# Kernel optimization log

Hardware: AMD Instinct MI355X
Metric: run time of the kernel (lower is better)

## Reference

```python
import jax, jax.numpy as jnp
import numpy as np

WS = (8, 8, 8)          # window_size (d, h, w) -- all equal
N_TOK = WS[0] * WS[1] * WS[2]   # 512
DIM = 192
HEADS = 6
HEAD_DIM = DIM // HEADS  # 32
B_ = 64                  # num_windows * batch (batch = 1)


def _build_rel_coords_table():
    # matches torch: meshgrid of arange(-(w-1), w) per axis, normalized, *8, signed log2
    r = np.arange(-(WS[0] - 1), WS[0], dtype=np.float32)
    tab = np.stack(np.meshgrid(r, r, r, indexing='ij'), axis=-1)[None]  # (1,15,15,15,3)
    tab = tab / (WS[0] - 1)
    tab = tab * 8.0
    tab = np.sign(tab) * np.log2(np.abs(tab) + 1.0) / np.log2(8.0)
    return tab.astype(np.float32)


def _build_rel_pos_index():
    c = np.arange(WS[0])
    coords = np.stack(np.meshgrid(c, c, c, indexing='ij'))          # (3, 8, 8, 8)
    flat = coords.reshape(3, -1)                                     # (3, N)
    rel = flat[:, :, None] - flat[:, None, :]                        # (3, N, N)
    rel = rel.transpose(1, 2, 0).copy()                              # (N, N, 3)
    rel += WS[0] - 1
    rel[:, :, 0] *= (2 * WS[1] - 1) * (2 * WS[2] - 1)
    rel[:, :, 1] *= 2 * WS[2] - 1
    return rel.sum(-1).astype(np.int32)                              # (N, N)


def setup_inputs() -> dict:
    key = jax.random.key(0)
    ks = jax.random.split(key, 8)
    x = jax.random.normal(ks[0], (B_, N_TOK, DIM), dtype=jnp.float32)
    # 0 / -inf style additive mask (use large negative finite for stability)
    m = jax.random.uniform(ks[1], (B_, N_TOK, N_TOK))
    mask = jnp.where(m < 0.1, jnp.float32(-1e4), jnp.float32(0.0))
    w_qkv = jax.random.normal(ks[2], (3 * DIM, DIM), dtype=jnp.float32) * (DIM ** -0.5)
    q_bias = jnp.zeros((DIM,), jnp.float32)
    v_bias = jnp.zeros((DIM,), jnp.float32)
    cpb_w1 = jax.random.normal(ks[3], (512, 3), dtype=jnp.float32) * 0.3
    cpb_b1 = jnp.zeros((512,), jnp.float32)
    cpb_w2 = jax.random.normal(ks[4], (HEADS, 512), dtype=jnp.float32) * 0.05
    rel_coords_table = jnp.asarray(_build_rel_coords_table())
    rel_pos_index = jnp.asarray(_build_rel_pos_index())
    return {"x": x, "mask": mask, "w_qkv": w_qkv, "q_bias": q_bias,
            "v_bias": v_bias, "cpb_w1": cpb_w1, "cpb_b1": cpb_b1,
            "cpb_w2": cpb_w2, "rel_coords_table": rel_coords_table,
            "rel_pos_index": rel_pos_index}


def reference(x, mask, w_qkv, q_bias, v_bias, cpb_w1, cpb_b1, cpb_w2,
              rel_coords_table, rel_pos_index):
    Bw, N, C = x.shape
    H, D = HEADS, HEAD_DIM
    # qkv projection with bias = cat(q_bias, zeros, v_bias)
    qkv_bias = jnp.concatenate([q_bias, jnp.zeros_like(v_bias), v_bias])
    qkv = x @ w_qkv.T + qkv_bias                       # (Bw, N, 3C)
    qkv = qkv.reshape(Bw, N, 3, H, D).transpose(2, 0, 3, 1, 4)
    q, k, v = qkv[0], qkv[1], qkv[2]                   # (Bw, H, N, D)
    # continuous position bias MLP: 3 -> 512 -> H
    tab = rel_coords_table.reshape(-1, 3)              # (3375, 3)
    tab = jax.nn.relu(tab @ cpb_w1.T + cpb_b1) @ cpb_w2.T  # (3375, H)
    bias = tab[rel_pos_index.reshape(-1)].reshape(N, N, H)
    bias = 16.0 * jax.nn.sigmoid(bias.transpose(2, 0, 1))  # (H, N, N)
    # SDPA with additive mask (standard 1/sqrt(D) scaling, as in forward_flash)
    scale = jnp.float32(1.0 / np.sqrt(D))
    scores = jnp.einsum('bhnd,bhmd->bhnm', q, k) * scale
    scores = scores + mask[:, None, :, :] + bias[None]
    attn = jax.nn.softmax(scores, axis=-1)
    out = jnp.einsum('bhnm,bhmd->bhnd', attn, v)       # (Bw, H, N, D)
    return out
```

## Files before the change

kernel.cpp:

```cpp
#include <hip/hip_runtime.h>
#include <hip/hip_bf16.h>


typedef __bf16 bf16x8 __attribute__((ext_vector_type(8)));
typedef __bf16 bf16x4v __attribute__((ext_vector_type(4)));
typedef float  f32x4  __attribute__((ext_vector_type(4)));
typedef _Float16 f16x4 __attribute__((ext_vector_type(4)));
typedef _Float16 f16x8 __attribute__((ext_vector_type(8)));
typedef unsigned uint2v __attribute__((ext_vector_type(2)));
typedef int int4v __attribute__((ext_vector_type(4)));
typedef unsigned long long u64;

#define LOG2E 1.4426950408889634f

__device__ __forceinline__ bf16x8 cvt2_bf16x8(f32x4 a, f32x4 b) {
  bf16x8 r;
  r[0] = (__bf16)a[0]; r[1] = (__bf16)a[1]; r[2] = (__bf16)a[2]; r[3] = (__bf16)a[3];
  r[4] = (__bf16)b[0]; r[5] = (__bf16)b[1]; r[6] = (__bf16)b[2]; r[7] = (__bf16)b[3];
  return r;
}

__device__ __forceinline__ unsigned pack2bf(float a, float b) {
  unsigned short ua = __builtin_bit_cast(unsigned short, (__bf16)a);
  unsigned short ub = __builtin_bit_cast(unsigned short, (__bf16)b);
  return (unsigned)ua | ((unsigned)ub << 16);
}

__device__ __forceinline__ bf16x8 frag_from_words(unsigned w0, unsigned w1,
                                                  unsigned w2, unsigned w3) {
  union { unsigned u[4]; bf16x8 v; } f;
  f.u[0] = w0; f.u[1] = w1; f.u[2] = w2; f.u[3] = w3;
  return f.v;
}

#define PREP_MB    2048
#define PREP_WCONV 108
#define PREP_CPB   3375
#define PREP_GRID  (PREP_MB + PREP_WCONV + PREP_CPB)

__global__ __launch_bounds__(256) void prep_kernel(
    const float* __restrict__ w, __bf16* __restrict__ wbf,
    const float* __restrict__ table, const float* __restrict__ w1,
    const float* __restrict__ b1, const float* __restrict__ w2,
    float* __restrict__ tab6,
    const float* __restrict__ m, u64* __restrict__ bits)
{
  __shared__ float red[4][6];
  int blk = blockIdx.x;
  if (blk < PREP_MB) {
    int li8 = threadIdx.x & 7;
    for (size_t t = (size_t)blk * 256 + threadIdx.x;
         t < 2097152ull; t += (size_t)PREP_MB * 256) {
      const float* mp = m + t * 8;
      f32x4 v0 = *(const f32x4*)mp;
      f32x4 v1 = *(const f32x4*)(mp + 4);
      unsigned byte =
          (v0[0] == 0.f ? 1u : 0u)  | (v0[1] == 0.f ? 2u : 0u) |
          (v0[2] == 0.f ? 4u : 0u)  | (v0[3] == 0.f ? 8u : 0u) |
          (v1[0] == 0.f ? 16u : 0u) | (v1[1] == 0.f ? 32u : 0u) |
          (v1[2] == 0.f ? 64u : 0u) | (v1[3] == 0.f ? 128u : 0u);
      u64 part = (u64)byte << (8 * li8);
      part |= __shfl_xor(part, 1);
      part |= __shfl_xor(part, 2);
      part |= __shfl_xor(part, 4);
      if (li8 == 0) {
        int w_ = (int)(t >> 3);
        int b = w_ >> 12, i = (w_ >> 3) & 511, jw = w_ & 7;
        bits[(((size_t)b * 8 + jw) << 9) + i] = part;
      }
    }
  } else if (blk < PREP_MB + PREP_WCONV) {
    int t = (blk - PREP_MB) * 256 + threadIdx.x;
    f32x4 v = *(const f32x4*)(w + (size_t)t * 4);
    bf16x4v o;
    o[0] = (__bf16)v[0]; o[1] = (__bf16)v[1]; o[2] = (__bf16)v[2]; o[3] = (__bf16)v[3];
    *(bf16x4v*)(wbf + (size_t)t * 4) = o;
  } else {
    int p = blk - PREP_MB - PREP_WCONV;
    float c0 = table[p * 3 + 0], c1 = table[p * 3 + 1], c2 = table[p * 3 + 2];
    float acc[6] = {0.f, 0.f, 0.f, 0.f, 0.f, 0.f};
#pragma unroll
    for (int jj = 0; jj < 2; ++jj) {
      int j = threadIdx.x + jj * 256;
      float hv = w1[j * 3 + 0] * c0 + w1[j * 3 + 1] * c1 + w1[j * 3 + 2] * c2 + b1[j];
      hv = fmaxf(hv, 0.0f);
#pragma unroll
      for (int t = 0; t < 6; ++t) acc[t] += w2[t * 512 + j] * hv;
    }
#pragma unroll
    for (int t = 0; t < 6; ++t) {
      acc[t] += __shfl_xor(acc[t], 1);
      acc[t] += __shfl_xor(acc[t], 2);
      acc[t] += __shfl_xor(acc[t], 4);
      acc[t] += __shfl_xor(acc[t], 8);
      acc[t] += __shfl_xor(acc[t], 16);
      acc[t] += __shfl_xor(acc[t], 32);
    }
    int wave = threadIdx.x >> 6;
    if ((threadIdx.x & 63) == 0)
#pragma unroll
      for (int t = 0; t < 6; ++t) red[wave][t] = acc[t];
    __syncthreads();
    if (threadIdx.x < 6) {
      int t = threadIdx.x;
      float s = red[0][t] + red[1][t] + red[2][t] + red[3][t];
      float sig = 16.0f / (1.0f + expf(-s));
      tab6[p * 8 + t] = sig * LOG2E;
    }
  }
}

#define MID_QKV  1024
#define MID_BIAS 342
#define MID_GRID (MID_QKV + MID_BIAS)

__global__ __launch_bounds__(192) void mid_kernel(
    const float* __restrict__ x,
    const __bf16* __restrict__ wbf,
    const float* __restrict__ qb,
    const float* __restrict__ vb,
    __bf16* __restrict__ Qo,
    __bf16* __restrict__ Ko,
    __bf16* __restrict__ Vt,
    const int* __restrict__ relidx,
    const float* __restrict__ tab6,
    _Float16* __restrict__ biasH)
{
  __shared__ __bf16 tile[2][32][72];
  if (blockIdx.x >= MID_QKV) {
    for (int q4 = (blockIdx.x - MID_QKV) * 192 + threadIdx.x; q4 < 65536;
         q4 += MID_BIAS * 192) {
      int ij = q4 * 4;
      int i = ij >> 9, p = ij & 511;
      int jblk = p >> 6, g = (p >> 4) & 3, kf = (p >> 2) & 3;
      int j = (jblk << 6) + kf * 16 + g * 4;
      int4v idx4 = *(const int4v*)(relidx + (i << 9) + j);
      float val[6][4];
#pragma unroll
      for (int u = 0; u < 4; ++u) {
        f32x4 lo = *(const f32x4*)(tab6 + (size_t)idx4[u] * 8);
        f32x4 hi = *(const f32x4*)(tab6 + (size_t)idx4[u] * 8 + 4);
        val[0][u] = lo[0]; val[1][u] = lo[1]; val[2][u] = lo[2];
        val[3][u] = lo[3]; val[4][u] = hi[0]; val[5][u] = hi[1];
      }
#pragma unroll
      for (int t6 = 0; t6 < 6; ++t6) {
        f16x4 o = {(_Float16)val[t6][0], (_Float16)val[t6][1],
                   (_Float16)val[t6][2], (_Float16)val[t6][3]};
        *(f16x4*)(biasH + (size_t)t6 * 262144 + ij) = o;
      }
    }
    return;
  }
  const float CQ = 0.17677669529663687f * LOG2E;
  int lane = threadIdx.x & 63, wave = threadIdx.x >> 6;
  int g = lane >> 4, li = lane & 15;
  int rowbase = blockIdx.x * 32;
  int b = rowbase >> 9, nbase = rowbase & 511;

  bf16x8 a[2][6];
#pragma unroll
  for (int mm = 0; mm < 2; ++mm)
#pragma unroll
    for (int k = 0; k < 6; ++k) {
      const float* xp = x + (size_t)(rowbase + mm * 16 + li) * 192 + k * 32 + 8 * g;
      f32x4 x0 = *(const f32x4*)xp;
      f32x4 x1 = *(const f32x4*)(xp + 4);
      a[mm][k] = cvt2_bf16x8(x0, x1);
    }

  for (int ncl = 0; ncl < 3; ++ncl) {
    int nc = wave * 3 + ncl;
    f32x4 acc[2][4];
#pragma unroll
    for (int n = 0; n < 4; ++n) {
      int r = nc * 64 + n * 16 + li;
      float bb = 0.0f;
      if (r < 192) bb = qb[r];
      else if (r >= 384) bb = vb[r - 384];
      f32x4 v = {bb, bb, bb, bb};
      acc[0][n] = v; acc[1][n] = v;
    }
#pragma unroll
    for (int k = 0; k < 6; ++k) {
#pragma unroll
      for (int n = 0; n < 4; ++n) {
        bf16x8 bf = *(const bf16x8*)(wbf + (size_t)(nc * 64 + n * 16 + li) * 192 + k * 32 + 8 * g);
        acc[0][n] = __builtin_amdgcn_mfma_f32_16x16x32_bf16(a[0][k], bf, acc[0][n], 0, 0, 0);
        acc[1][n] = __builtin_amdgcn_mfma_f32_16x16x32_bf16(a[1][k], bf, acc[1][n], 0, 0, 0);
      }
    }
    if (wave < 2) {
      float scale = (wave == 0) ? CQ : 1.0f;
#pragma unroll
      for (int n = 0; n < 4; ++n)
#pragma unroll
        for (int mm = 0; mm < 2; ++mm)
#pragma unroll
          for (int t = 0; t < 4; ++t)
            tile[wave][mm * 16 + 4 * g + t][n * 16 + li] = (__bf16)(acc[mm][n][t] * scale);
      int tok = lane & 31, hh = lane >> 5;
      int h = (nc * 2 + hh) % 6;
      __bf16* base = (wave == 0) ? Qo : Ko;
      __bf16* dst = base + ((size_t)(b * 6 + h) * 512 + nbase + tok) * 32;
#pragma unroll
      for (int kq = 0; kq < 4; ++kq)
        *(bf16x8*)(dst + kq * 8) = *(const bf16x8*)&tile[wave][tok][hh * 32 + kq * 8];
    } else {
#pragma unroll
      for (int n = 0; n < 4; ++n) {
        int rr = nc * 64 + n * 16 + li - 384, h = rr >> 5, d = rr & 31;
#pragma unroll
        for (int mm = 0; mm < 2; ++mm) {
          int nn = nbase + mm * 16 + 4 * g;
          bf16x4v pk;
#pragma unroll
          for (int t = 0; t < 4; ++t) pk[t] = (__bf16)acc[mm][n][t];
          *(bf16x4v*)(Vt + ((size_t)(b * 6 + h) * 32 + d) * 512 + nn) = pk;
        }
      }
    }
  }
}

__global__ __launch_bounds__(256, 3) void attn_kernel(
    const u64* __restrict__ bits,
    const _Float16* __restrict__ biasH,
    const __bf16* __restrict__ Qw,
    const __bf16* __restrict__ Kw,
    const __bf16* __restrict__ Vt,
    float* __restrict__ out)
{
  int hw = blockIdx.x;
  int xcd = hw & 7, seq = hw >> 3;
  int h = seq >> 4;
  int r = seq & 15;
  int b = xcd * 8 + (r >> 1);
  int qt = r & 1;
  int lane = threadIdx.x & 63, wave = threadIdx.x >> 6;
  int g = lane >> 4, li = lane & 15;
  int qbase = qt * 256 + wave * 64;
  int bh = b * 6 + h;
  int gsh = 4 * g;

  const __bf16* Qb = Qw + (size_t)bh * 16384;
  const __bf16* Kb = Kw + (size_t)bh * 16384;
  const __bf16* Vb = Vt + (size_t)bh * 16384;
  const _Float16* biasb = biasH + (size_t)h * 262144 + g * 16;
  const u64* bitsb = bits + (size_t)b * 4096;

  bf16x8 qfrag[4];
#pragma unroll
  for (int qf = 0; qf < 4; ++qf)
    qfrag[qf] = *(const bf16x8*)(Qb + (qbase + qf * 16 + li) * 32 + 8 * g);

  f32x4 oacc[4][2] = {};
  float l_part[4] = {0.f, 0.f, 0.f, 0.f};

  for (int kb = 0; kb < 8; ++kb) {
    int j64 = kb * 64;
    u64 mb[4];
#pragma unroll
    for (int qf = 0; qf < 4; ++qf)
      mb[qf] = bitsb[(kb << 9) + qbase + qf * 16 + li] >> gsh;
    bf16x8 kfr[4];
#pragma unroll
    for (int kf = 0; kf < 4; ++kf)
      kfr[kf] = *(const bf16x8*)(Kb + (j64 + kf * 16 + li) * 32 + 8 * g);
    bf16x8 vfr[2][2];
#pragma unroll
    for (int df = 0; df < 2; ++df)
#pragma unroll
      for (int c = 0; c < 2; ++c)
        vfr[df][c] = *(const bf16x8*)(Vb + (df * 16 + li) * 512 + j64 + c * 32 + 8 * g);
    f16x8 hv8[4][2];
#pragma unroll
    for (int qf = 0; qf < 4; ++qf) {
      const _Float16* bp = biasb + (size_t)(qbase + qf * 16 + li) * 512 + j64;
      hv8[qf][0] = *(const f16x8*)(bp);
      hv8[qf][1] = *(const f16x8*)(bp + 8);
    }

#pragma unroll
    for (int c = 0; c < 2; ++c) {
      unsigned lo[4][2], hi[4][2];
#pragma unroll
      for (int kfl = 0; kfl < 2; ++kfl) {
        int kf = c * 2 + kfl;
        const int hsel = kf >> 1, hoff = (kf & 1) * 4;
#pragma unroll
        for (int qf = 0; qf < 4; ++qf) {
          f16x8 hb = hv8[qf][hsel];
          f32x4 ci = {(float)hb[hoff], (float)hb[hoff + 1],
                      (float)hb[hoff + 2], (float)hb[hoff + 3]};
          f32x4 s = __builtin_amdgcn_mfma_f32_16x16x32_bf16(kfr[kf], qfrag[qf], ci, 0, 0, 0);
          unsigned nib = (unsigned)(mb[qf] >> (kf * 16)) & 15u;
          float p0 = (nib & 1u) ? __builtin_amdgcn_exp2f(s[0]) : 0.0f;
          float p1 = (nib & 2u) ? __builtin_amdgcn_exp2f(s[1]) : 0.0f;
          float p2 = (nib & 4u) ? __builtin_amdgcn_exp2f(s[2]) : 0.0f;
          float p3 = (nib & 8u) ? __builtin_amdgcn_exp2f(s[3]) : 0.0f;
          l_part[qf] += (p0 + p1) + (p2 + p3);
          lo[qf][kfl] = pack2bf(p0, p1);
          hi[qf][kfl] = pack2bf(p2, p3);
        }
      }
#pragma unroll
      for (int qf = 0; qf < 4; ++qf) {
        uint2v sl = __builtin_amdgcn_permlane32_swap(lo[qf][0], lo[qf][1], 0, 0);
        uint2v wl = __builtin_amdgcn_permlane16_swap(sl.x, sl.y, 0, 0);
        uint2v sh = __builtin_amdgcn_permlane32_swap(hi[qf][0], hi[qf][1], 0, 0);
        uint2v wh = __builtin_amdgcn_permlane16_swap(sh.x, sh.y, 0, 0);
        bf16x8 pf = frag_from_words(wl.x, wh.x, wl.y, wh.y);
#pragma unroll
        for (int df = 0; df < 2; ++df)
          oacc[qf][df] = __builtin_amdgcn_mfma_f32_16x16x32_bf16(vfr[df][c], pf, oacc[qf][df], 0, 0, 0);
      }
    }
  }

#pragma unroll
  for (int qf = 0; qf < 4; ++qf) {
    float l = l_part[qf];
    l += __shfl_xor(l, 16);
    l += __shfl_xor(l, 32);
    float linv = 1.0f / l;
#pragma unroll
    for (int df = 0; df < 2; ++df) {
      float* op = out + ((size_t)bh * 512 + qbase + qf * 16 + li) * 32 + df * 16 + 4 * g;
      f32x4 r2 = oacc[qf][df] * linv;
      *(f32x4*)op = r2;
    }
  }
}

extern "C" void kernel_launch(void* const* d_in, const int* in_sizes, int n_in,
                              void* d_out, int out_size, void* d_ws, size_t ws_size,
                              hipStream_t stream) {
  const float* x    = (const float*)d_in[0];
  const float* mask = (const float*)d_in[1];
  const float* wqkv = (const float*)d_in[2];
  const float* qb   = (const float*)d_in[3];
  const float* vb   = (const float*)d_in[4];
  const float* w1   = (const float*)d_in[5];
  const float* b1   = (const float*)d_in[6];
  const float* w2   = (const float*)d_in[7];
  const float* tbl  = (const float*)d_in[8];
  const int*   ridx = (const int*)d_in[9];
  float* out = (float*)d_out;

  char* ws = (char*)d_ws;
  float*    tab6  = (float*)(ws);
  _Float16* biasH = (_Float16*)(ws + 131072);
  u64*      bits  = (u64*)(ws + 131072 + 3145728);
  __bf16*   wbf   = (__bf16*)(ws + 131072 + 3145728 + 2097152);
  __bf16*   Q     = (__bf16*)(ws + 131072 + 3145728 + 2097152 + 262144);
  __bf16*   K     = Q + (size_t)64 * 6 * 512 * 32;
  __bf16*   Vt    = K + (size_t)64 * 6 * 512 * 32;

  prep_kernel<<<PREP_GRID, 256, 0, stream>>>(wqkv, wbf, tbl, w1, b1, w2, tab6,
                                             mask, bits);
  mid_kernel<<<MID_GRID, 192, 0, stream>>>(x, wbf, qb, vb, Q, K, Vt,
                                           ridx, tab6, biasH);
  attn_kernel<<<768, 256, 0, stream>>>(bits, biasH, Q, K, Vt, out);
}
```

Before: 119.9 us.

## Compute softmax row sums via MFMA with ones and branchless bitmask masking

Replaces the per-lane scalar accumulation of softmax denominators (and the final cross-lane shuffles) with an extra MFMA that multiplies the bf16 probability fragment by a ones matrix, so row sums come out of the matrix unit. Mask handling switches from conditional selects on a 64-bit word to sign-extended bit masks ANDed into the exp2 results, using 32-bit halves. It also raises wave priority around the compute loop with s_setprio. This trades VALU adds and shuffles for one more MFMA per fragment, and the denominators are now summed from bf16-rounded probabilities, which slightly changes numerics.

New measurement: 111.3 us (median of 3 runs). 1.08x faster.

```diff
diff --git a/kernel.cpp b/kernel.cpp
--- a/kernel.cpp
+++ b/kernel.cpp
@@ -254,15 +254,23 @@
   for (int qf = 0; qf < 4; ++qf)
     qfrag[qf] = *(const bf16x8*)(Qb + (qbase + qf * 16 + li) * 32 + 8 * g);
 
+  union { unsigned short us[8]; bf16x8 v; } onesu;
+#pragma unroll
+  for (int i = 0; i < 8; ++i) onesu.us[i] = 0x3F80;
+  bf16x8 ones = onesu.v;
+
   f32x4 oacc[4][2] = {};
-  float l_part[4] = {0.f, 0.f, 0.f, 0.f};
+  f32x4 lacc[4] = {};
 
   for (int kb = 0; kb < 8; ++kb) {
     int j64 = kb * 64;
-    u64 mb[4];
-#pragma unroll
-    for (int qf = 0; qf < 4; ++qf)
-      mb[qf] = bitsb[(kb << 9) + qbase + qf * 16 + li] >> gsh;
+    unsigned mbl[4], mbh[4];
+#pragma unroll
+    for (int qf = 0; qf < 4; ++qf) {
+      u64 m64 = bitsb[(kb << 9) + qbase + qf * 16 + li] >> gsh;
+      mbl[qf] = (unsigned)m64;
+      mbh[qf] = (unsigned)(m64 >> 32);
+    }
     bf16x8 kfr[4];
 #pragma unroll
     for (int kf = 0; kf < 4; ++kf)
@@ -281,6 +289,7 @@
       hv8[qf][1] = *(const f16x8*)(bp + 8);
     }
 
+    __builtin_amdgcn_s_setprio(1);
 #pragma unroll
     for (int c = 0; c < 2; ++c) {
       unsigned lo[4][2], hi[4][2];
@@ -288,18 +297,26 @@
       for (int kfl = 0; kfl < 2; ++kfl) {
         int kf = c * 2 + kfl;
         const int hsel = kf >> 1, hoff = (kf & 1) * 4;
+        const int bb0 = (kf & 1) * 16;
 #pragma unroll
         for (int qf = 0; qf < 4; ++qf) {
           f16x8 hb = hv8[qf][hsel];
           f32x4 ci = {(float)hb[hoff], (float)hb[hoff + 1],
                       (float)hb[hoff + 2], (float)hb[hoff + 3]};
           f32x4 s = __builtin_amdgcn_mfma_f32_16x16x32_bf16(kfr[kf], qfrag[qf], ci, 0, 0, 0);
-          unsigned nib = (unsigned)(mb[qf] >> (kf * 16)) & 15u;
-          float p0 = (nib & 1u) ? __builtin_amdgcn_exp2f(s[0]) : 0.0f;
-          float p1 = (nib & 2u) ? __builtin_amdgcn_exp2f(s[1]) : 0.0f;
-          float p2 = (nib & 4u) ? __builtin_amdgcn_exp2f(s[2]) : 0.0f;
-          float p3 = (nib & 8u) ? __builtin_amdgcn_exp2f(s[3]) : 0.0f;
-          l_part[qf] += (p0 + p1) + (p2 + p3);
+          unsigned mword = hsel ? mbh[qf] : mbl[qf];
+          unsigned m0 = (unsigned)((int)(mword << (31 - (bb0 + 0))) >> 31);
+          unsigned m1 = (unsigned)((int)(mword << (31 - (bb0 + 1))) >> 31);
+          unsigned m2 = (unsigned)((int)(mword << (31 - (bb0 + 2))) >> 31);
+          unsigned m3 = (unsigned)((int)(mword << (31 - (bb0 + 3))) >> 31);
+          float p0 = __builtin_bit_cast(float,
+              __builtin_bit_cast(unsigned, __builtin_amdgcn_exp2f(s[0])) & m0);
+          float p1 = __builtin_bit_cast(float,
+              __builtin_bit_cast(unsigned, __builtin_amdgcn_exp2f(s[1])) & m1);
+          float p2 = __builtin_bit_cast(float,
+              __builtin_bit_cast(unsigned, __builtin_amdgcn_exp2f(s[2])) & m2);
+          float p3 = __builtin_bit_cast(float,
+              __builtin_bit_cast(unsigned, __builtin_amdgcn_exp2f(s[3])) & m3);
           lo[qf][kfl] = pack2bf(p0, p1);
           hi[qf][kfl] = pack2bf(p2, p3);
         }
@@ -311,19 +328,17 @@
         uint2v sh = __builtin_amdgcn_permlane32_swap(hi[qf][0], hi[qf][1], 0, 0);
         uint2v wh = __builtin_amdgcn_permlane16_swap(sh.x, sh.y, 0, 0);
         bf16x8 pf = frag_from_words(wl.x, wh.x, wl.y, wh.y);
-#pragma unroll
-        for (int df = 0; df < 2; ++df)
-          oacc[qf][df] = __builtin_amdgcn_mfma_f32_16x16x32_bf16(vfr[df][c], pf, oacc[qf][df], 0, 0, 0);
-      }
-    }
+        oacc[qf][0] = __builtin_amdgcn_mfma_f32_16x16x32_bf16(vfr[0][c], pf, oacc[qf][0], 0, 0, 0);
+        oacc[qf][1] = __builtin_amdgcn_mfma_f32_16x16x32_bf16(vfr[1][c], pf, oacc[qf][1], 0, 0, 0);
+        lacc[qf]    = __builtin_amdgcn_mfma_f32_16x16x32_bf16(ones, pf, lacc[qf], 0, 0, 0);
+      }
+    }
+    __builtin_amdgcn_s_setprio(0);
   }
 
 #pragma unroll
   for (int qf = 0; qf < 4; ++qf) {
-    float l = l_part[qf];
-    l += __shfl_xor(l, 16);
-    l += __shfl_xor(l, 32);
-    float linv = 1.0f / l;
+    float linv = 1.0f / lacc[qf][0];
 #pragma unroll
     for (int df = 0; df < 2; ++df) {
       float* op = out + ((size_t)bh * 512 + qbase + qf * 16 + li) * 32 + df * 16 + 4 * g;
```
